# Performance work log

Hardware: AMD Instinct MI355X
Metric: run time of the kernel (lower is better)

Reference implementation:

```python
import jax, jax.numpy as jnp
import numpy as np

B, N, D, OUT = 8192, 256, 128, 10  # batch, input_dim (sites), bond_dim, output_dim
LOCAL = 2  # local physical dimension (hardcoded in source)


def setup_inputs() -> dict:
    key = jax.random.key(0)
    ks = jax.random.split(key, 6)
    scale = 1.0 / np.sqrt(D)  # stable variant of source's 0.1 init (keeps 256-site product O(1))
    x = jax.random.normal(ks[0], (B, N), dtype=jnp.float32)
    first = jax.random.normal(ks[1], (1, LOCAL, D), dtype=jnp.float32) * scale   # site 0: (1,2,D)
    mid = jax.random.normal(ks[2], (N - 2, D, LOCAL, D), dtype=jnp.float32) * scale  # sites 1..N-2
    last = jax.random.normal(ks[3], (D, LOCAL, 1), dtype=jnp.float32) * scale    # site N-1: (D,2,1)
    w = jax.random.normal(ks[4], (OUT, 1), dtype=jnp.float32) * 0.1  # nn.Linear(1, OUT) weight
    b = jnp.zeros((OUT,), dtype=jnp.float32)                          # nn.Linear(1, OUT) bias
    return {"x": x, "first": first, "mid": mid, "last": last, "w": w, "b": b}


def _feature_map(x):
    # per-sample min/max normalization over the feature axis, then (cos, sin) embedding
    x_min = jnp.min(x, axis=1, keepdims=True)
    x_max = jnp.max(x, axis=1, keepdims=True)
    x_norm = (x - x_min) / (x_max - x_min + 1e-6)
    ang = (np.pi / 2) * x_norm
    return jnp.stack([jnp.cos(ang), jnp.sin(ang)], axis=2)  # [B, N, 2]


def reference(x, first, mid, last, w, b):
    phi = _feature_map(x)  # [B, N, 2]
    # site 0: left[b, r] = sum_d first[0, d, r] * phi[b, 0, d]
    left = jnp.einsum('dr,bd->br', first[0], phi[:, 0])  # [B, D]
    # sites 1..N-2 via scan: left <- sum_{l,d} left[b,l] * M[l,d,r] * phi[b,i,d]
    phi_mid = jnp.swapaxes(phi[:, 1:-1], 0, 1)  # [N-2, B, 2]

    def step(left, inputs):
        M, p = inputs  # M: [D, 2, D], p: [B, 2]
        left = jnp.einsum('bl,ldr,bd->br', left, M, p)
        return left, None

    left, _ = jax.lax.scan(step, left, (mid, phi_mid))  # [B, D]
    # last site: scalar[b] = sum_{l,d} left[b,l] * last[l,d,0] * phi[b,N-1,d]
    scalar = jnp.einsum('bl,ld,bd->b', left, last[:, :, 0], phi[:, -1])  # [B]
    # nn.Linear(1, OUT): logits = scalar * w^T + b
    logits = scalar[:, None] * w[:, 0][None, :] + b  # [B, OUT]
    return logits
```

## Files before the change

### kernel.cpp

```cpp
#include <hip/hip_runtime.h>


typedef _Float16 v8h __attribute__((ext_vector_type(8)));
typedef _Float16 h2  __attribute__((ext_vector_type(2)));
typedef float    v4f __attribute__((ext_vector_type(4)));

#define PI_HALF 1.5707963267948966f
#define SITE_U4 4096
#define TOFF_U4 (127*4096)
#define LOUT_F32 (2*TOFF_U4*4)
#define ROUT_F32 (LOUT_F32 + 8192*128)
#define PHI_S 160

union U4H8 { uint4 u; v8h h; };

__device__ __forceinline__ v4f mfma16h(uint4 a, uint4 b, v4f c){
  U4H8 ua, ub; ua.u = a; ub.u = b;
  return __builtin_amdgcn_mfma_f32_16x16x32_f16(ua.h, ub.h, c, 0, 0, 0);
}
__device__ __forceinline__ unsigned pack2h(float lo, float hi){
  h2 p; p[0] = (_Float16)lo; p[1] = (_Float16)hi;
  return __builtin_bit_cast(unsigned, p);
}
__device__ __forceinline__ unsigned short f16b(float v){
  return __builtin_bit_cast(unsigned short, (_Float16)v);
}

__global__ __launch_bounds__(256) void repack_mid(const float* __restrict__ mid,
                                                  unsigned short* __restrict__ wsB){
  const int bid = blockIdx.x;
  if (bid < 508){
    int idx  = bid * 256 + threadIdx.x;
    int lg   = idx & 15;
    int nt   = (idx >> 4) & 7;
    int kt   = (idx >> 7) & 3;
    int d    = (idx >> 9) & 1;
    int site = idx >> 10;
    int q    = lg >> 2;
    int n0   = 16*nt + 4*(lg & 3);
    const float* src = mid + ((size_t)(site*128 + 32*kt + 8*q)*2 + d)*128 + n0;
    float V[8][4];
    #pragma unroll
    for (int j = 0; j < 8; ++j){
      float4 a = *(const float4*)(src + (size_t)j*256);
      V[j][0]=a.x; V[j][1]=a.y; V[j][2]=a.z; V[j][3]=a.w;
    }
    uint4* dst = (uint4*)wsB + ((((size_t)site*2 + d)*4 + kt)*8 + nt)*64
               + 16*q + 4*(lg & 3);
    #pragma unroll
    for (int t = 0; t < 4; ++t){
      uint4 o;
      o.x = pack2h(V[0][t], V[1][t]);
      o.y = pack2h(V[2][t], V[3][t]);
      o.z = pack2h(V[4][t], V[5][t]);
      o.w = pack2h(V[6][t], V[7][t]);
      dst[t] = o;
    }
  } else {
    int idx  = (bid - 508) * 256 + threadIdx.x;
    int lg   = idx & 15;
    int kt   = (idx >> 4) & 3;
    int am   = (idx >> 6) & 7;
    int d    = (idx >> 9) & 1;
    int srel = idx >> 10;
    int site = 127 + srel;
    int q    = lg >> 2;
    int m0   = 16*am + 4*(lg & 3);
    int k0   = 32*kt + 8*q;
    uint4* dst = (uint4*)wsB + TOFF_U4
               + ((((size_t)srel*2 + d)*8 + am)*4 + kt)*64 + 16*q + 4*(lg & 3);
    #pragma unroll
    for (int mp = 0; mp < 4; ++mp){
      const float* src = mid + ((size_t)((site*128 + m0 + mp)*2) + d)*128 + k0;
      float4 a = *(const float4*)(src);
      float4 b = *(const float4*)(src + 4);
      uint4 o;
      o.x = pack2h(a.x, a.y);
      o.y = pack2h(a.z, a.w);
      o.z = pack2h(b.x, b.y);
      o.w = pack2h(b.z, b.w);
      dst[mp] = o;
    }
  }
}

__global__ __launch_bounds__(512, 2) void mps_main(
    const float* __restrict__ x,
    const float* __restrict__ first,
    const unsigned short* __restrict__ wsBv,
    const float* __restrict__ lastw,
    float* __restrict__ ws_out)
{
  __shared__ unsigned phiL[128*PHI_S];
  __shared__ unsigned Ast[2*16*64*4];

  const int tid  = threadIdx.x;
  const int bid  = blockIdx.x;
  const int dir  = bid >> 7;
  const int rg   = bid & 127;
  const int w    = tid >> 6;
  const int lane = tid & 63;
  const int r    = lane & 15;
  const int q    = lane >> 4;
  const int rh   = r >> 3;
  const int rowbase = rg * 64;
  const int physL = lane ^ ((lane >> 3) & 7);

  {
    const int row = tid >> 3;
    const int c   = tid & 7;
    const float4* xp = (const float4*)(x + (size_t)(rowbase + row) * 256 + c*32);
    float xv[32];
    float vmin = 3.0e38f, vmax = -3.0e38f;
    #pragma unroll
    for (int cc = 0; cc < 8; ++cc){
      float4 u = xp[cc];
      xv[cc*4+0] = u.x; xv[cc*4+1] = u.y; xv[cc*4+2] = u.z; xv[cc*4+3] = u.w;
      vmin = fminf(vmin, fminf(fminf(u.x,u.y), fminf(u.z,u.w)));
      vmax = fmaxf(vmax, fmaxf(fmaxf(u.x,u.y), fmaxf(u.z,u.w)));
    }
    #pragma unroll
    for (int m = 1; m < 8; m <<= 1){
      vmin = fminf(vmin, __shfl_xor(vmin, m));
      vmax = fmaxf(vmax, __shfl_xor(vmax, m));
    }
    const float sc = PI_HALF / (vmax - vmin + 1e-6f);
    const bool mine = dir ? (c >= 4) : (c < 4);
    if (mine){
      const int s0 = 32*c - (dir ? 128 : 0);
      #pragma unroll
      for (int j = 0; j < 32; ++j){
        float a = (xv[j] - vmin) * sc;
        phiL[(s0 + j)*PHI_S + row] = pack2h(__cosf(a), __sinf(a));
      }
    }
  }
  __syncthreads();

  uint4 F0[8], F1[8];
  if (dir == 0){
    const int mt = w >> 1;
    #pragma unroll
    for (int cc = 0; cc < 2; ++cc){
      const int kt = 2*(w & 1) + cc;
      const int m  = 16*mt + r;
      h2 p0 = __builtin_bit_cast(h2, phiL[0*PHI_S + m]);
      const float c0 = (float)p0[0], s0 = (float)p0[1];
      uint4 o; unsigned ow[4];
      #pragma unroll
      for (int jp = 0; jp < 4; ++jp){
        const int k = 32*kt + 8*q + 2*jp;
        float v0 = first[k]  *c0 + first[128+k]  *s0;
        float v1 = first[k+1]*c0 + first[128+k+1]*s0;
        ow[jp] = pack2h(v0, v1);
      }
      o.x=ow[0]; o.y=ow[1]; o.z=ow[2]; o.w=ow[3];
      *(uint4*)&Ast[((mt*4 + kt)*64 + physL)*4] = o;
    }
    const uint4* bp = (const uint4*)wsBv;
    #pragma unroll
    for (int pl = 0; pl < 2; ++pl)
      #pragma unroll
      for (int kt = 0; kt < 4; ++kt)
        F0[pl*4+kt] = bp[(size_t)((pl*4 + kt)*8 + w)*64 + lane];
  } else {
    const int kt = w >> 1;
    #pragma unroll
    for (int cc = 0; cc < 2; ++cc){
      const int nt = 2*(w & 1) + cc;
      const int n  = 16*nt + r;
      h2 p5 = __builtin_bit_cast(h2, phiL[127*PHI_S + n]);
      const float cb = (float)p5[0], sb = (float)p5[1];
      uint4 o; unsigned ow[4];
      #pragma unroll
      for (int jp = 0; jp < 4; ++jp){
        const int k = 32*kt + 8*q + 2*jp;
        float2 g0 = *(const float2*)(lastw + 2*k);
        float2 g1 = *(const float2*)(lastw + 2*(k+1));
        ow[jp] = pack2h(g0.x*cb + g0.y*sb, g1.x*cb + g1.y*sb);
      }
      o.x=ow[0]; o.y=ow[1]; o.z=ow[2]; o.w=ow[3];
      *(uint4*)&Ast[((kt*4 + nt)*64 + physL)*4] = o;
    }
    const uint4* bp = (const uint4*)wsBv + TOFF_U4 + (size_t)126 * SITE_U4;
    #pragma unroll
    for (int pl = 0; pl < 2; ++pl)
      #pragma unroll
      for (int kt = 0; kt < 4; ++kt)
        F0[pl*4+kt] = bp[(size_t)((pl*8 + w)*4 + kt)*64 + lane];
  }

  float* Lout = ws_out + LOUT_F32;
  float* Rout = ws_out + ROUT_F32;

  auto body = [&](int s, uint4 (&Fc)[8], uint4 (&Fn)[8]){
    __syncthreads();

    if (dir == 0){
      const int soff = (s < 126) ? (s + 1) : 0;
      const uint4* bp = (const uint4*)wsBv + (size_t)soff * SITE_U4;
      #pragma unroll
      for (int pl = 0; pl < 2; ++pl)
        #pragma unroll
        for (int kt = 0; kt < 4; ++kt)
          Fn[pl*4+kt] = bp[(size_t)((pl*4 + kt)*8 + w)*64 + lane];
    } else {
      const int srel = (s < 126) ? (125 - s) : 0;
      const uint4* bp = (const uint4*)wsBv + TOFF_U4 + (size_t)srel * SITE_U4;
      #pragma unroll
      for (int pl = 0; pl < 2; ++pl)
        #pragma unroll
        for (int kt = 0; kt < 4; ++kt)
          Fn[pl*4+kt] = bp[(size_t)((pl*8 + w)*4 + kt)*64 + lane];
    }

    v4f acc[4][2] = {};
    const unsigned* Sb = &Ast[(s & 1) * 4096];
    #pragma unroll
    for (int kt = 0; kt < 4; ++kt){
      if (dir == 0){
        #pragma unroll
        for (int mt = 0; mt < 4; ++mt){
          uint4 a = *(const uint4*)&Sb[((mt*4 + kt)*64 + physL)*4];
          acc[mt][0] = mfma16h(a, Fc[0*4+kt], acc[mt][0]);
          acc[mt][1] = mfma16h(a, Fc[1*4+kt], acc[mt][1]);
        }
      } else {
        #pragma unroll
        for (int nt = 0; nt < 4; ++nt){
          uint4 b = *(const uint4*)&Sb[((kt*4 + nt)*64 + physL)*4];
          acc[nt][0] = mfma16h(Fc[0*4+kt], b, acc[nt][0]);
          acc[nt][1] = mfma16h(Fc[1*4+kt], b, acc[nt][1]);
        }
      }
    }

    if (s < 126){
      unsigned short* Wb = (unsigned short*)&Ast[((s+1) & 1) * 4096];
      if (dir == 0){
        const int X  = 4*(w & 1) + 2*rh + (q >> 1);
        const int S0 = 32*(w & 1) + 16*rh + 4*q;
        #pragma unroll
        for (int mt = 0; mt < 4; ++mt){
          uint4 phiu = *(const uint4*)&phiL[(s+1)*PHI_S + 16*mt + 4*q];
          const unsigned pr[4] = {phiu.x, phiu.y, phiu.z, phiu.w};
          const int base = (mt*4 + (w >> 1))*512;
          #pragma unroll
          for (int reg = 0; reg < 4; ++reg){
            h2 ph = __builtin_bit_cast(h2, pr[reg]);
            float v = (float)ph[0]*acc[mt][0][reg] + (float)ph[1]*acc[mt][1][reg];
            Wb[base + ((S0 + reg) ^ X)*8 + (r & 7)] = f16b(v);
          }
        }
      } else {
        const int ps = 254 - s;
        const int X  = 4*(w & 1) + 2*(q >> 1) + rh;
        const int S  = (32*(w & 1) + 16*(q >> 1) + r) ^ X;
        #pragma unroll
        for (int nt = 0; nt < 4; ++nt){
          h2 ph = __builtin_bit_cast(h2, phiL[(ps-128)*PHI_S + 16*nt + r]);
          const float cb = (float)ph[0], sb = (float)ph[1];
          const int base = ((w >> 1)*4 + nt)*512 + S*8 + 4*(q & 1);
          #pragma unroll
          for (int reg = 0; reg < 4; ++reg){
            float v = cb*acc[nt][0][reg] + sb*acc[nt][1][reg];
            Wb[base + reg] = f16b(v);
          }
        }
      }
    } else {
      if (dir == 0){
        #pragma unroll
        for (int mt = 0; mt < 4; ++mt){
          uint4 phiu = *(const uint4*)&phiL[127*PHI_S + 16*mt + 4*q];
          const unsigned pr[4] = {phiu.x, phiu.y, phiu.z, phiu.w};
          #pragma unroll
          for (int reg = 0; reg < 4; ++reg){
            h2 ph = __builtin_bit_cast(h2, pr[reg]);
            float v = (float)ph[0]*acc[mt][0][reg] + (float)ph[1]*acc[mt][1][reg];
            Lout[(size_t)(rowbase + 16*mt + 4*q + reg)*128 + 16*w + r] = v;
          }
        }
      } else {
        #pragma unroll
        for (int nt = 0; nt < 4; ++nt){
          h2 ph = __builtin_bit_cast(h2, phiL[0*PHI_S + 16*nt + r]);
          const float cb = (float)ph[0], sb = (float)ph[1];
          float4 vv;
          vv.x = cb*acc[nt][0][0] + sb*acc[nt][1][0];
          vv.y = cb*acc[nt][0][1] + sb*acc[nt][1][1];
          vv.z = cb*acc[nt][0][2] + sb*acc[nt][1][2];
          vv.w = cb*acc[nt][0][3] + sb*acc[nt][1][3];
          *(float4*)(Rout + (size_t)rg*8192 + (16*nt + r)*128 + 16*w + 4*q) = vv;
        }
      }
    }
  };

  #pragma unroll 1
  for (int s = 0; s < 126; s += 2){
    body(s,     F0, F1);
    body(s + 1, F1, F0);
  }
  body(126, F0, F1);
}

__global__ __launch_bounds__(256) void combine(const float* __restrict__ ws,
                                               const float* __restrict__ wlin,
                                               const float* __restrict__ blin,
                                               float* __restrict__ out){
  const int t   = blockIdx.x * 256 + threadIdx.x;
  const int row = t >> 2;
  const int c   = t & 3;
  const float* Lp = ws + LOUT_F32 + (size_t)row*128 + c*32;
  const float* Rp = ws + ROUT_F32 + (size_t)(row >> 6)*8192 + (row & 63)*128 + c*32;
  float s = 0.0f;
  #pragma unroll
  for (int i = 0; i < 8; ++i){
    float4 a = ((const float4*)Lp)[i];
    float4 b = ((const float4*)Rp)[i];
    s += a.x*b.x + a.y*b.y + a.z*b.z + a.w*b.w;
  }
  s += __shfl_xor(s, 1);
  s += __shfl_xor(s, 2);
  if (c == 0){
    #pragma unroll
    for (int o = 0; o < 10; ++o)
      out[(size_t)row*10 + o] = s*wlin[o] + blin[o];
  }
}

extern "C" void kernel_launch(void* const* d_in, const int* in_sizes, int n_in,
                              void* d_out, int out_size, void* d_ws, size_t ws_size,
                              hipStream_t stream){
  (void)in_sizes; (void)n_in; (void)out_size; (void)ws_size;
  const float* x     = (const float*)d_in[0];
  const float* first = (const float*)d_in[1];
  const float* mid   = (const float*)d_in[2];
  const float* lastw = (const float*)d_in[3];
  const float* wlin  = (const float*)d_in[4];
  const float* blin  = (const float*)d_in[5];
  float* o            = (float*)d_out;
  unsigned short* wsB = (unsigned short*)d_ws;

  hipLaunchKernelGGL(repack_mid, dim3(1016), dim3(256), 0, stream, mid, wsB);
  hipLaunchKernelGGL(mps_main,   dim3(256),  dim3(512), 0, stream,
                     x, first, wsB, lastw, (float*)d_ws);
  hipLaunchKernelGGL(combine,    dim3(128),  dim3(256), 0, stream,
                     (const float*)d_ws, wlin, blin, o);
}
```

Before: 267.3 us.

## Precompute pairwise site-tensor products to halve the sequential MPS chain

A new preprocessing kernel multiplies adjacent mid-site tensors for all four physical index pairs (d,e) into fp16 MFMA-ready fragments. The main kernel then advances two sites per step, with four accumulators combined using products of the two sites' phi values, so the serial loop runs about half as many steps with larger MFMA bursts. This shortens the latency-bound sequential chain at the cost of a heavier repack that does matrix products, twice the fragment registers, and an extra fp16 rounding of the product tensors.

Result: slower. 333.6 us (+24.8%).

```diff
diff --git a/kernel.cpp b/kernel.cpp
--- a/kernel.cpp
+++ b/kernel.cpp
@@ -6,11 +6,14 @@
 typedef float    v4f __attribute__((ext_vector_type(4)));
 
 #define PI_HALF 1.5707963267948966f
-#define SITE_U4 4096
-#define TOFF_U4 (127*4096)
-#define LOUT_F32 (2*TOFF_U4*4)
-#define ROUT_F32 (LOUT_F32 + 8192*128)
-#define PHI_S 160
+#define STEP_U4    8192
+#define FWD_SGL_U4 516096
+#define BWD_U4     520192
+#define BWD_SGL_U4 1036288
+#define WS_U4      1040384
+#define LOUT_F32   (WS_U4*4)
+#define ROUT_F32   (LOUT_F32 + 8192*128)
+#define PHI_S 66
 
 union U4H8 { uint4 u; v8h h; };
 
@@ -26,60 +29,108 @@
   return __builtin_bit_cast(unsigned short, (_Float16)v);
 }
 
-__global__ __launch_bounds__(256) void repack_mid(const float* __restrict__ mid,
-                                                  unsigned short* __restrict__ wsB){
-  const int bid = blockIdx.x;
-  if (bid < 508){
-    int idx  = bid * 256 + threadIdx.x;
-    int lg   = idx & 15;
-    int nt   = (idx >> 4) & 7;
-    int kt   = (idx >> 7) & 3;
-    int d    = (idx >> 9) & 1;
-    int site = idx >> 10;
-    int q    = lg >> 2;
-    int n0   = 16*nt + 4*(lg & 3);
-    const float* src = mid + ((size_t)(site*128 + 32*kt + 8*q)*2 + d)*128 + n0;
-    float V[8][4];
-    #pragma unroll
-    for (int j = 0; j < 8; ++j){
-      float4 a = *(const float4*)(src + (size_t)j*256);
-      V[j][0]=a.x; V[j][1]=a.y; V[j][2]=a.z; V[j][3]=a.w;
-    }
-    uint4* dst = (uint4*)wsB + ((((size_t)site*2 + d)*4 + kt)*8 + nt)*64
-               + 16*q + 4*(lg & 3);
-    #pragma unroll
-    for (int t = 0; t < 4; ++t){
-      uint4 o;
-      o.x = pack2h(V[0][t], V[1][t]);
-      o.y = pack2h(V[2][t], V[3][t]);
-      o.z = pack2h(V[4][t], V[5][t]);
-      o.w = pack2h(V[6][t], V[7][t]);
-      dst[t] = o;
-    }
+__global__ __launch_bounds__(256) void repack_products(const float* __restrict__ mid,
+                                                       unsigned short* __restrict__ wsB){
+  const int wg  = blockIdx.x;
+  const int tid = threadIdx.x;
+  const int lg  = tid & 15, l3 = lg & 3, q = lg >> 2;
+  const int oi  = tid >> 4;
+  const int ot  = oi >> 1;
+  const int h   = oi & 1;
+
+  __shared__ unsigned Afr[8192];
+  __shared__ unsigned Bfr[8192];
+
+  auto stageP1 = [&](unsigned* dst, const float* src, bool isA){
+    #pragma unroll
+    for (int c = 0; c < 2; ++c){
+      const int kt = 2*h + c;
+      const int k0 = 32*kt + 8*q;
+      #pragma unroll
+      for (int mp = 0; mp < 4; ++mp){
+        const int outer = 16*ot + 4*l3 + mp;
+        const float* s = src + (size_t)outer*256 + k0;
+        float4 a = *(const float4*)s;
+        float4 b = *(const float4*)(s + 4);
+        const int frag = isA ? (ot*4 + kt) : (kt*8 + ot);
+        unsigned* o = dst + (frag*64 + 16*q + 4*l3 + mp)*4;
+        o[0]=pack2h(a.x,a.y); o[1]=pack2h(a.z,a.w);
+        o[2]=pack2h(b.x,b.y); o[3]=pack2h(b.z,b.w);
+      }
+    }
+  };
+  auto stageP2 = [&](unsigned* dst, const float* src, bool isA){
+    #pragma unroll
+    for (int c = 0; c < 2; ++c){
+      const int kt = 2*h + c;
+      const int o0 = 16*ot + 4*l3;
+      float V[8][4];
+      #pragma unroll
+      for (int jj = 0; jj < 8; ++jj){
+        const int k = 32*kt + 8*q + jj;
+        float4 a = *(const float4*)(src + (size_t)k*256 + o0);
+        V[jj][0]=a.x; V[jj][1]=a.y; V[jj][2]=a.z; V[jj][3]=a.w;
+      }
+      const int frag = isA ? (ot*4 + kt) : (kt*8 + ot);
+      #pragma unroll
+      for (int t = 0; t < 4; ++t){
+        unsigned* o = dst + (frag*64 + 16*q + 4*l3 + t)*4;
+        o[0]=pack2h(V[0][t],V[1][t]); o[1]=pack2h(V[2][t],V[3][t]);
+        o[2]=pack2h(V[4][t],V[5][t]); o[3]=pack2h(V[6][t],V[7][t]);
+      }
+    }
+  };
+
+  if (wg >= 504){
+    const int ss = wg - 504, half = ss >> 1, d = ss & 1;
+    if (half == 0){
+      unsigned* dst = (unsigned*)((uint4*)wsB + FWD_SGL_U4 + d*2048);
+      stageP2(dst, mid + (size_t)126*32768 + d*128, false);
+    } else {
+      unsigned* dst = (unsigned*)((uint4*)wsB + BWD_SGL_U4 + d*2048);
+      stageP1(dst, mid + (size_t)127*32768 + d*128, true);
+    }
+    return;
+  }
+
+  const bool isf = wg < 252;
+  const int idx  = isf ? wg : wg - 252;
+  const int step = idx >> 2, de = idx & 3, d = de >> 1, e = de & 1;
+  const int j    = isf ? 2*step : 252 - 2*step;
+
+  if (isf){
+    stageP1(Afr, mid + (size_t)j*32768 + d*128, true);
+    stageP2(Bfr, mid + (size_t)(j+1)*32768 + e*128, false);
   } else {
-    int idx  = (bid - 508) * 256 + threadIdx.x;
-    int lg   = idx & 15;
-    int kt   = (idx >> 4) & 3;
-    int am   = (idx >> 6) & 7;
-    int d    = (idx >> 9) & 1;
-    int srel = idx >> 10;
-    int site = 127 + srel;
-    int q    = lg >> 2;
-    int m0   = 16*am + 4*(lg & 3);
-    int k0   = 32*kt + 8*q;
-    uint4* dst = (uint4*)wsB + TOFF_U4
-               + ((((size_t)srel*2 + d)*8 + am)*4 + kt)*64 + 16*q + 4*(lg & 3);
-    #pragma unroll
-    for (int mp = 0; mp < 4; ++mp){
-      const float* src = mid + ((size_t)((site*128 + m0 + mp)*2) + d)*128 + k0;
-      float4 a = *(const float4*)(src);
-      float4 b = *(const float4*)(src + 4);
-      uint4 o;
-      o.x = pack2h(a.x, a.y);
-      o.y = pack2h(a.z, a.w);
-      o.z = pack2h(b.x, b.y);
-      o.w = pack2h(b.z, b.w);
-      dst[mp] = o;
+    stageP2(Afr, mid + (size_t)(j+1)*32768 + e*128, true);
+    stageP1(Bfr, mid + (size_t)j*32768 + d*128, false);
+  }
+  __syncthreads();
+
+  const int w = tid >> 6, lane = tid & 63, r = lane & 15, qq = lane >> 4;
+  v4f acc[2][8] = {};
+  #pragma unroll
+  for (int kt = 0; kt < 4; ++kt){
+    uint4 a0 = *(const uint4*)&Afr[(((2*w+0)*4 + kt)*64 + lane)*4];
+    uint4 a1 = *(const uint4*)&Afr[(((2*w+1)*4 + kt)*64 + lane)*4];
+    #pragma unroll
+    for (int nt = 0; nt < 8; ++nt){
+      uint4 b = *(const uint4*)&Bfr[((kt*8 + nt)*64 + lane)*4];
+      acc[0][nt] = mfma16h(a0, b, acc[0][nt]);
+      acc[1][nt] = mfma16h(a1, b, acc[1][nt]);
+    }
+  }
+
+  const size_t dstU4 = (isf ? 0 : BWD_U4) + (size_t)step*STEP_U4 + de*2048;
+  uint2* gp = (uint2*)((uint4*)wsB + dstU4);
+  #pragma unroll
+  for (int i = 0; i < 2; ++i){
+    const int lane_i = 16*(2*i + (qq >> 1)) + r;
+    #pragma unroll
+    for (int nt = 0; nt < 8; ++nt){
+      unsigned w0 = pack2h(acc[i][nt][0], acc[i][nt][1]);
+      unsigned w1 = pack2h(acc[i][nt][2], acc[i][nt][3]);
+      gp[((w*8 + nt)*64 + lane_i)*2 + (qq & 1)] = make_uint2(w0, w1);
     }
   }
 }
@@ -137,7 +188,7 @@
   }
   __syncthreads();
 
-  uint4 F0[8], F1[8];
+  uint4 F0[16], F1[16];
   if (dir == 0){
     const int mt = w >> 1;
     #pragma unroll
@@ -157,12 +208,6 @@
       o.x=ow[0]; o.y=ow[1]; o.z=ow[2]; o.w=ow[3];
       *(uint4*)&Ast[((mt*4 + kt)*64 + physL)*4] = o;
     }
-    const uint4* bp = (const uint4*)wsBv;
-    #pragma unroll
-    for (int pl = 0; pl < 2; ++pl)
-      #pragma unroll
-      for (int kt = 0; kt < 4; ++kt)
-        F0[pl*4+kt] = bp[(size_t)((pl*4 + kt)*8 + w)*64 + lane];
   } else {
     const int kt = w >> 1;
     #pragma unroll
@@ -182,127 +227,163 @@
       o.x=ow[0]; o.y=ow[1]; o.z=ow[2]; o.w=ow[3];
       *(uint4*)&Ast[((kt*4 + nt)*64 + physL)*4] = o;
     }
-    const uint4* bp = (const uint4*)wsBv + TOFF_U4 + (size_t)126 * SITE_U4;
-    #pragma unroll
-    for (int pl = 0; pl < 2; ++pl)
+  }
+  {
+    const uint4* bp = (const uint4*)wsBv + (dir ? BWD_U4 : 0);
+    #pragma unroll
+    for (int de = 0; de < 4; ++de)
       #pragma unroll
       for (int kt = 0; kt < 4; ++kt)
-        F0[pl*4+kt] = bp[(size_t)((pl*8 + w)*4 + kt)*64 + lane];
+        F0[de*4+kt] = bp[(size_t)de*2048 + (kt*8 + w)*64 + lane];
   }
 
   float* Lout = ws_out + LOUT_F32;
   float* Rout = ws_out + ROUT_F32;
 
-  auto body = [&](int s, uint4 (&Fc)[8], uint4 (&Fn)[8]){
+  auto body = [&](int p, uint4 (&Fc)[16], uint4 (&Fn)[16]){
     __syncthreads();
 
-    if (dir == 0){
-      const int soff = (s < 126) ? (s + 1) : 0;
-      const uint4* bp = (const uint4*)wsBv + (size_t)soff * SITE_U4;
-      #pragma unroll
-      for (int pl = 0; pl < 2; ++pl)
+    if (p < 62){
+      const uint4* bp = (const uint4*)wsBv + (dir ? BWD_U4 : 0) + (size_t)(p+1)*STEP_U4;
+      #pragma unroll
+      for (int de = 0; de < 4; ++de)
         #pragma unroll
         for (int kt = 0; kt < 4; ++kt)
-          Fn[pl*4+kt] = bp[(size_t)((pl*4 + kt)*8 + w)*64 + lane];
-    } else {
-      const int srel = (s < 126) ? (125 - s) : 0;
-      const uint4* bp = (const uint4*)wsBv + TOFF_U4 + (size_t)srel * SITE_U4;
-      #pragma unroll
-      for (int pl = 0; pl < 2; ++pl)
-        #pragma unroll
-        for (int kt = 0; kt < 4; ++kt)
-          Fn[pl*4+kt] = bp[(size_t)((pl*8 + w)*4 + kt)*64 + lane];
-    }
-
-    v4f acc[4][2] = {};
-    const unsigned* Sb = &Ast[(s & 1) * 4096];
-    #pragma unroll
-    for (int kt = 0; kt < 4; ++kt){
-      if (dir == 0){
-        #pragma unroll
-        for (int mt = 0; mt < 4; ++mt){
-          uint4 a = *(const uint4*)&Sb[((mt*4 + kt)*64 + physL)*4];
-          acc[mt][0] = mfma16h(a, Fc[0*4+kt], acc[mt][0]);
-          acc[mt][1] = mfma16h(a, Fc[1*4+kt], acc[mt][1]);
-        }
-      } else {
-        #pragma unroll
-        for (int nt = 0; nt < 4; ++nt){
-          uint4 b = *(const uint4*)&Sb[((kt*4 + nt)*64 + physL)*4];
-          acc[nt][0] = mfma16h(Fc[0*4+kt], b, acc[nt][0]);
-          acc[nt][1] = mfma16h(Fc[1*4+kt], b, acc[nt][1]);
-        }
-      }
-    }
-
-    if (s < 126){
-      unsigned short* Wb = (unsigned short*)&Ast[((s+1) & 1) * 4096];
-      if (dir == 0){
-        const int X  = 4*(w & 1) + 2*rh + (q >> 1);
-        const int S0 = 32*(w & 1) + 16*rh + 4*q;
-        #pragma unroll
-        for (int mt = 0; mt < 4; ++mt){
-          uint4 phiu = *(const uint4*)&phiL[(s+1)*PHI_S + 16*mt + 4*q];
-          const unsigned pr[4] = {phiu.x, phiu.y, phiu.z, phiu.w};
-          const int base = (mt*4 + (w >> 1))*512;
-          #pragma unroll
-          for (int reg = 0; reg < 4; ++reg){
-            h2 ph = __builtin_bit_cast(h2, pr[reg]);
-            float v = (float)ph[0]*acc[mt][0][reg] + (float)ph[1]*acc[mt][1][reg];
-            Wb[base + ((S0 + reg) ^ X)*8 + (r & 7)] = f16b(v);
-          }
-        }
-      } else {
-        const int ps = 254 - s;
-        const int X  = 4*(w & 1) + 2*(q >> 1) + rh;
-        const int S  = (32*(w & 1) + 16*(q >> 1) + r) ^ X;
-        #pragma unroll
-        for (int nt = 0; nt < 4; ++nt){
-          h2 ph = __builtin_bit_cast(h2, phiL[(ps-128)*PHI_S + 16*nt + r]);
-          const float cb = (float)ph[0], sb = (float)ph[1];
-          const int base = ((w >> 1)*4 + nt)*512 + S*8 + 4*(q & 1);
-          #pragma unroll
-          for (int reg = 0; reg < 4; ++reg){
-            float v = cb*acc[nt][0][reg] + sb*acc[nt][1][reg];
-            Wb[base + reg] = f16b(v);
-          }
-        }
-      }
+          Fn[de*4+kt] = bp[(size_t)de*2048 + (kt*8 + w)*64 + lane];
     } else {
       if (dir == 0){
-        #pragma unroll
-        for (int mt = 0; mt < 4; ++mt){
-          uint4 phiu = *(const uint4*)&phiL[127*PHI_S + 16*mt + 4*q];
-          const unsigned pr[4] = {phiu.x, phiu.y, phiu.z, phiu.w};
+        const uint4* bp = (const uint4*)wsBv + FWD_SGL_U4;
+        #pragma unroll
+        for (int d = 0; d < 2; ++d)
           #pragma unroll
-          for (int reg = 0; reg < 4; ++reg){
-            h2 ph = __builtin_bit_cast(h2, pr[reg]);
-            float v = (float)ph[0]*acc[mt][0][reg] + (float)ph[1]*acc[mt][1][reg];
-            Lout[(size_t)(rowbase + 16*mt + 4*q + reg)*128 + 16*w + r] = v;
-          }
+          for (int kt = 0; kt < 4; ++kt)
+            Fn[d*4+kt] = bp[(size_t)d*2048 + (kt*8 + w)*64 + lane];
+      } else {
+        const uint4* bp = (const uint4*)wsBv + BWD_SGL_U4;
+        #pragma unroll
+        for (int d = 0; d < 2; ++d)
+          #pragma unroll
+          for (int kt = 0; kt < 4; ++kt)
+            Fn[d*4+kt] = bp[(size_t)d*2048 + (w*4 + kt)*64 + lane];
+      }
+    }
+
+    v4f acc[4][4] = {};
+    const unsigned* Sb = &Ast[(p & 1) * 4096];
+    #pragma unroll
+    for (int kt = 0; kt < 4; ++kt){
+      uint4 sfr[4];
+      #pragma unroll
+      for (int i = 0; i < 4; ++i){
+        const int fi = (dir == 0) ? (i*4 + kt) : (kt*4 + i);
+        sfr[i] = *(const uint4*)&Sb[(fi*64 + physL)*4];
+      }
+      #pragma unroll
+      for (int de = 0; de < 4; ++de)
+        #pragma unroll
+        for (int i = 0; i < 4; ++i)
+          acc[i][de] = (dir == 0) ? mfma16h(sfr[i], Fc[de*4+kt], acc[i][de])
+                                  : mfma16h(Fc[de*4+kt], sfr[i], acc[i][de]);
+    }
+
+    unsigned short* Wb = (unsigned short*)&Ast[((p+1) & 1) * 4096];
+    if (dir == 0){
+      const int X  = 4*(w & 1) + 2*rh + (q >> 1);
+      const int S0 = 32*(w & 1) + 16*rh + 4*q;
+      const int i1 = 2*p + 1, i2 = 2*p + 2;
+      #pragma unroll
+      for (int mt = 0; mt < 4; ++mt){
+        uint4 pA = *(const uint4*)&phiL[i1*PHI_S + 16*mt + 4*q];
+        uint4 pB = *(const uint4*)&phiL[i2*PHI_S + 16*mt + 4*q];
+        const unsigned prA[4] = {pA.x,pA.y,pA.z,pA.w};
+        const unsigned prB[4] = {pB.x,pB.y,pB.z,pB.w};
+        const int base = (mt*4 + (w >> 1))*512;
+        #pragma unroll
+        for (int reg = 0; reg < 4; ++reg){
+          h2 hA = __builtin_bit_cast(h2, prA[reg]);
+          h2 hB = __builtin_bit_cast(h2, prB[reg]);
+          const float c1 = (float)hA[0], s1 = (float)hA[1];
+          const float c2 = (float)hB[0], s2 = (float)hB[1];
+          float v = (c1*c2)*acc[mt][0][reg] + (c1*s2)*acc[mt][1][reg]
+                  + (s1*c2)*acc[mt][2][reg] + (s1*s2)*acc[mt][3][reg];
+          Wb[base + ((S0 + reg) ^ X)*8 + (r & 7)] = f16b(v);
         }
-      } else {
-        #pragma unroll
-        for (int nt = 0; nt < 4; ++nt){
-          h2 ph = __builtin_bit_cast(h2, phiL[0*PHI_S + 16*nt + r]);
-          const float cb = (float)ph[0], sb = (float)ph[1];
-          float4 vv;
-          vv.x = cb*acc[nt][0][0] + sb*acc[nt][1][0];
-          vv.y = cb*acc[nt][0][1] + sb*acc[nt][1][1];
-          vv.z = cb*acc[nt][0][2] + sb*acc[nt][1][2];
-          vv.w = cb*acc[nt][0][3] + sb*acc[nt][1][3];
-          *(float4*)(Rout + (size_t)rg*8192 + (16*nt + r)*128 + 16*w + 4*q) = vv;
+      }
+    } else {
+      const int X = 4*(w & 1) + 2*(q >> 1) + rh;
+      const int S = (32*(w & 1) + 16*(q >> 1) + r) ^ X;
+      const int i1 = 125 - 2*p, i2 = 126 - 2*p;
+      #pragma unroll
+      for (int nt = 0; nt < 4; ++nt){
+        h2 p1 = __builtin_bit_cast(h2, phiL[i1*PHI_S + 16*nt + r]);
+        h2 p2 = __builtin_bit_cast(h2, phiL[i2*PHI_S + 16*nt + r]);
+        const float k00 = (float)p1[0]*(float)p2[0];
+        const float k01 = (float)p1[0]*(float)p2[1];
+        const float k10 = (float)p1[1]*(float)p2[0];
+        const float k11 = (float)p1[1]*(float)p2[1];
+        const int base = ((w >> 1)*4 + nt)*512 + S*8 + 4*(q & 1);
+        #pragma unroll
+        for (int reg = 0; reg < 4; ++reg){
+          float v = k00*acc[nt][0][reg] + k01*acc[nt][1][reg]
+                  + k10*acc[nt][2][reg] + k11*acc[nt][3][reg];
+          Wb[base + reg] = f16b(v);
         }
       }
     }
   };
 
   #pragma unroll 1
-  for (int s = 0; s < 126; s += 2){
-    body(s,     F0, F1);
-    body(s + 1, F1, F0);
-  }
-  body(126, F0, F1);
+  for (int p = 0; p < 62; p += 2){
+    body(p,     F0, F1);
+    body(p + 1, F1, F0);
+  }
+  body(62, F0, F1);
+
+  {
+    __syncthreads();
+    v4f acc[4][2] = {};
+    const unsigned* Sb = &Ast[4096];
+    #pragma unroll
+    for (int kt = 0; kt < 4; ++kt){
+      uint4 sfr[4];
+      #pragma unroll
+      for (int i = 0; i < 4; ++i){
+        const int fi = (dir == 0) ? (i*4 + kt) : (kt*4 + i);
+        sfr[i] = *(const uint4*)&Sb[(fi*64 + physL)*4];
+      }
+      #pragma unroll
+      for (int d = 0; d < 2; ++d)
+        #pragma unroll
+        for (int i = 0; i < 4; ++i)
+          acc[i][d] = (dir == 0) ? mfma16h(sfr[i], F1[d*4+kt], acc[i][d])
+                                 : mfma16h(F1[d*4+kt], sfr[i], acc[i][d]);
+    }
+    if (dir == 0){
+      #pragma unroll
+      for (int mt = 0; mt < 4; ++mt){
+        uint4 pA = *(const uint4*)&phiL[127*PHI_S + 16*mt + 4*q];
+        const unsigned pr[4] = {pA.x,pA.y,pA.z,pA.w};
+        #pragma unroll
+        for (int reg = 0; reg < 4; ++reg){
+          h2 ph = __builtin_bit_cast(h2, pr[reg]);
+          float v = (float)ph[0]*acc[mt][0][reg] + (float)ph[1]*acc[mt][1][reg];
+          Lout[(size_t)(rowbase + 16*mt + 4*q + reg)*128 + 16*w + r] = v;
+        }
+      }
+    } else {
+      #pragma unroll
+      for (int nt = 0; nt < 4; ++nt){
+        h2 ph = __builtin_bit_cast(h2, phiL[0*PHI_S + 16*nt + r]);
+        const float cb = (float)ph[0], sb = (float)ph[1];
+        float4 vv;
+        vv.x = cb*acc[nt][0][0] + sb*acc[nt][1][0];
+        vv.y = cb*acc[nt][0][1] + sb*acc[nt][1][1];
+        vv.z = cb*acc[nt][0][2] + sb*acc[nt][1][2];
+        vv.w = cb*acc[nt][0][3] + sb*acc[nt][1][3];
+        *(float4*)(Rout + (size_t)rg*8192 + (16*nt + r)*128 + 16*w + 4*q) = vv;
+      }
+    }
+  }
 }
 
 __global__ __launch_bounds__(256) void combine(const float* __restrict__ ws,
@@ -343,9 +424,9 @@
   float* o            = (float*)d_out;
   unsigned short* wsB = (unsigned short*)d_ws;
 
-  hipLaunchKernelGGL(repack_mid, dim3(1016), dim3(256), 0, stream, mid, wsB);
-  hipLaunchKernelGGL(mps_main,   dim3(256),  dim3(512), 0, stream,
+  hipLaunchKernelGGL(repack_products, dim3(508), dim3(256), 0, stream, mid, wsB);
+  hipLaunchKernelGGL(mps_main,        dim3(256), dim3(512), 0, stream,
                      x, first, wsB, lastw, (float*)d_ws);
-  hipLaunchKernelGGL(combine,    dim3(128),  dim3(256), 0, stream,
+  hipLaunchKernelGGL(combine,         dim3(128), dim3(256), 0, stream,
                      (const float*)d_ws, wlin, blin, o);
 }
```
